# Kernel optimization log

Hardware: AMD Instinct MI355X
Metric: run time of the kernel (lower is better)

The kernel has to match this reference:

```python
import jax, jax.numpy as jnp
import numpy as np

B, N, DIM = 32, 577, 768   # N = num_patches + 1
H, DH = 12, 64             # heads, dim_head; inner_dim = H*DH = 768
NEG = -987654321.0         # LSA diagonal mask value from the source


def setup_inputs() -> dict:
    key = jax.random.key(0)
    ks = jax.random.split(key, 5)
    inner = H * DH
    base_scale = DH ** -0.5
    return {
        "x": jax.random.normal(ks[0], (B, N, DIM), dtype=jnp.float32),
        "W_qkv": jax.random.normal(ks[1], (DIM, inner * 3), dtype=jnp.float32) * (DIM ** -0.5),
        "scale": base_scale * (1.0 + 0.01 * jax.random.normal(ks[2], (H,), dtype=jnp.float32)),
        "W_out": jax.random.normal(ks[3], (inner, DIM), dtype=jnp.float32) * (inner ** -0.5),
        "b_out": jnp.zeros((DIM,), dtype=jnp.float32),
    }


def reference(x, W_qkv, scale, W_out, b_out):
    b, n, _ = x.shape
    qkv = x @ W_qkv                                   # [b, n, 3*H*DH]
    q, k, v = jnp.split(qkv, 3, axis=-1)
    to_heads = lambda t: t.reshape(b, n, H, DH).transpose(0, 2, 1, 3)  # b h n d
    q, k, v = to_heads(q), to_heads(k), to_heads(v)
    # per-head learnable scale (LSA)
    dots = jnp.einsum('bhid,bhjd->bhij', q, k) * scale[None, :, None, None]
    # mask self-attention diagonal (eye scatter in the torch source)
    eye = jnp.eye(n, dtype=bool)
    dots = jnp.where(eye[None, None], NEG, dots)
    attn = jax.nn.softmax(dots, axis=-1)
    out = jnp.einsum('bhij,bhjd->bhid', attn, v)      # b h n d
    out = out.transpose(0, 2, 1, 3).reshape(b, n, H * DH)
    return out @ W_out + b_out
```

## Files before the change

kernel.cpp:

```cpp
#include <hip/hip_runtime.h>


typedef _Float16 half8  __attribute__((ext_vector_type(8)));
typedef _Float16 h4f    __attribute__((ext_vector_type(4)));
typedef __fp16   hv2    __attribute__((ext_vector_type(2)));
typedef __fp16   hv4    __attribute__((ext_vector_type(4)));
typedef float    floatx4 __attribute__((ext_vector_type(4)));

#define MTOT   18464
#define NEG_V  (-987654321.0f)
#define VTS    584

__device__ __forceinline__ void gl_lds16(const _Float16* g, _Float16* l) {
    __builtin_amdgcn_global_load_lds(
        (const __attribute__((address_space(1))) unsigned int*)g,
        (__attribute__((address_space(3))) unsigned int*)l,
        16, 0, 0);
}

__global__ __launch_bounds__(256) void cvt_x(const float* __restrict__ x,
                                             _Float16* __restrict__ x16) {
    const size_t idx = ((size_t)blockIdx.x * 256 + threadIdx.x) * 8;
    half8 h = {};
    if (idx < (size_t)MTOT * 768) {
        float4 a = *(const float4*)(x + idx);
        float4 b = *(const float4*)(x + idx + 4);
        h[0] = (_Float16)a.x; h[1] = (_Float16)a.y;
        h[2] = (_Float16)a.z; h[3] = (_Float16)a.w;
        h[4] = (_Float16)b.x; h[5] = (_Float16)b.y;
        h[6] = (_Float16)b.z; h[7] = (_Float16)b.w;
    }
    *(half8*)(x16 + idx) = h;
}

__global__ __launch_bounds__(256) void transpose_w(const float* __restrict__ src,
                                                   _Float16* __restrict__ dst,
                                                   int K, int Ncol) {
    __shared__ float tile[32][33];
    const int n0 = blockIdx.x * 32, k0 = blockIdx.y * 32;
    const int tx = threadIdx.x & 31, ty = threadIdx.x >> 5;
    for (int i = 0; i < 32; i += 8)
        tile[ty + i][tx] = src[(size_t)(k0 + ty + i) * Ncol + (n0 + tx)];
    __syncthreads();
    for (int i = 0; i < 32; i += 8)
        dst[(size_t)(n0 + ty + i) * K + (k0 + tx)] = (_Float16)tile[tx][ty + i];
}

__global__ __launch_bounds__(512, 4) void gemm_qkv(const _Float16* __restrict__ x16,
                                                   const _Float16* __restrict__ wT,
                                                   const float* __restrict__ scale,
                                                   _Float16* __restrict__ qg,
                                                   _Float16* __restrict__ kg,
                                                   _Float16* __restrict__ vT) {
    __shared__ _Float16 As[2][128 * 32];
    __shared__ _Float16 Bs[2][256 * 32];
    const int m0 = blockIdx.x * 128, n0 = blockIdx.y * 256;
    const int tid = threadIdx.x;
    const int lane = tid & 63, wv = tid >> 6;
    const int wrow = wv >> 2, wcol = wv & 3;
    const int lr = lane & 15, lq = lane >> 4;

    const int ra  = tid >> 2,            ca  = (tid & 3) * 8;
    const int rb0 = tid >> 2,            cb0 = (tid & 3) * 8;
    const int rb1 = (512 + tid) >> 2,    cb1 = (tid & 3) * 8;

    floatx4 acc[4][4];
    const floatx4 fz = {0.f, 0.f, 0.f, 0.f};
    for (int i = 0; i < 4; ++i)
        for (int j = 0; j < 4; ++j) acc[i][j] = fz;

    #define STAGE_QKV(ki, bf)                                                     \
        do {                                                                      \
            const int kk_ = (ki) * 32;                                            \
            gl_lds16(x16 + (size_t)(m0 + ra) * 768 + kk_ + ca, &As[bf][wv*64*8]); \
            gl_lds16(wT + (size_t)(n0 + rb0) * 768 + kk_ + cb0, &Bs[bf][wv*64*8]);\
            gl_lds16(wT + (size_t)(n0 + rb1) * 768 + kk_ + cb1,                   \
                     &Bs[bf][(512 + wv*64) * 8]);                                 \
        } while (0)

    STAGE_QKV(0, 0);
    for (int ki = 0; ki < 24; ++ki) {
        const int bf = ki & 1;
        if (ki < 23) {
            STAGE_QKV(ki + 1, bf ^ 1);
            asm volatile("s_waitcnt vmcnt(3)" ::: "memory");
        } else {
            asm volatile("s_waitcnt vmcnt(0)" ::: "memory");
        }
        asm volatile("s_barrier" ::: "memory");

        half8 af[4], bfr[4];
        #pragma unroll
        for (int i = 0; i < 4; ++i)
            af[i] = *(const half8*)&As[bf][(wrow * 64 + i * 16 + lr) * 32 + lq * 8];
        #pragma unroll
        for (int j = 0; j < 4; ++j)
            bfr[j] = *(const half8*)&Bs[bf][(wcol * 64 + j * 16 + lr) * 32 + lq * 8];
        #pragma unroll
        for (int i = 0; i < 4; ++i)
            #pragma unroll
            for (int j = 0; j < 4; ++j)
                acc[i][j] = __builtin_amdgcn_mfma_f32_16x16x32_f16(af[i], bfr[j], acc[i][j], 0, 0, 0);

        asm volatile("s_waitcnt lgkmcnt(0)\n\ts_barrier" ::: "memory");
    }
    #undef STAGE_QKV

    const int cbase = n0 + wcol * 64;
    const int which = cbase / 768;
    const int h = (cbase - which * 768) >> 6;
    const float qsc = (which == 0) ? scale[h] * 1.4426950408889634f : 1.0f;
    #pragma unroll
    for (int j = 0; j < 4; ++j) {
        const int d = j * 16 + lr;
        #pragma unroll
        for (int i = 0; i < 4; ++i)
            #pragma unroll
            for (int r = 0; r < 4; ++r) {
                const int row = m0 + wrow * 64 + i * 16 + lq * 4 + r;
                if (row >= MTOT) continue;
                const unsigned bb = (unsigned)row / 577u;
                const unsigned nn = (unsigned)row - bb * 577u;
                const _Float16 val = (_Float16)(acc[i][j][r] * qsc);
                const size_t head = (size_t)(bb * 12 + h);
                if (which == 0)      qg[(head * 577 + nn) * 64 + d] = val;
                else if (which == 1) kg[(head * 577 + nn) * 64 + d] = val;
                else                 vT[(head * 64 + d) * VTS + nn] = val;
            }
    }
}

__global__ __launch_bounds__(256) void attn_kernel(const _Float16* __restrict__ qg,
                                                   const _Float16* __restrict__ kg,
                                                   const _Float16* __restrict__ vT,
                                                   _Float16* __restrict__ Og) {
    __shared__ __align__(16) _Float16 Ks[64 * 64];
    __shared__ __align__(16) _Float16 Vs[64 * 64];
    const int qt = blockIdx.x, h = blockIdx.y, b = blockIdx.z;
    const int tid = threadIdx.x, lane = tid & 63, wv = tid >> 6;
    const int lr = lane & 15, lq = lane >> 4;
    const size_t head = (size_t)(b * 12 + h);
    const _Float16* qh = qg + head * 577 * 64;
    const _Float16* kh = kg + head * 577 * 64;
    const _Float16* vh = vT + head * 64 * VTS;
    const int q0 = qt * 128;
    const int xs = lq ^ (lr & 7), xs4 = xs ^ 4;

    half8 bq[2][2];
    #pragma unroll
    for (int st = 0; st < 2; ++st) {
        const int qi = q0 + st * 64 + wv * 16 + lr;
        const int qc = qi < 577 ? qi : 576;
        bq[st][0] = *(const half8*)(qh + (size_t)qc * 64 + lq * 8);
        bq[st][1] = *(const half8*)(qh + (size_t)qc * 64 + 32 + lq * 8);
    }

    const floatx4 fz = {0.f, 0.f, 0.f, 0.f};
    floatx4 ot[2][4];
    #pragma unroll
    for (int st = 0; st < 2; ++st)
        #pragma unroll
        for (int c = 0; c < 4; ++c) ot[st][c] = fz;
    float sacc[2] = {0.f, 0.f};

    for (int kt = 0; kt < 10; ++kt) {
        const int j0 = kt * 64;
        __syncthreads();
        #pragma unroll
        for (int t = 0; t < 2; ++t) {
            const int c = t * 256 + wv * 64 + lane;
            const int row = c >> 3, cl = (c & 7) ^ (row & 7);
            gl_lds16(kh + (size_t)(j0 + row) * 64 + cl * 8,
                     Ks + (t * 256 + wv * 64) * 8);
            gl_lds16(vh + (size_t)row * VTS + j0 + cl * 8,
                     Vs + (t * 256 + wv * 64) * 8);
        }
        __syncthreads();

        half8 ak[4][2];
        #pragma unroll
        for (int ct = 0; ct < 4; ++ct) {
            const int base = (ct * 16 + lr) * 64;
            ak[ct][0] = *(const half8*)&Ks[base + xs * 8];
            ak[ct][1] = *(const half8*)&Ks[base + xs4 * 8];
        }

        floatx4 s[2][4];
        #pragma unroll
        for (int st = 0; st < 2; ++st)
            #pragma unroll
            for (int ct = 0; ct < 4; ++ct) {
                floatx4 t = __builtin_amdgcn_mfma_f32_16x16x32_f16(ak[ct][0], bq[st][0], fz, 0, 0, 0);
                s[st][ct] = __builtin_amdgcn_mfma_f32_16x16x32_f16(ak[ct][1], bq[st][1], t, 0, 0, 0);
            }

        if (kt == 9) {
            #pragma unroll
            for (int st = 0; st < 2; ++st) {
                s[st][0][0] = (lq == 0) ? s[st][0][0] : -INFINITY;
                s[st][0][1] = -INFINITY; s[st][0][2] = -INFINITY; s[st][0][3] = -INFINITY;
                #pragma unroll
                for (int ct = 1; ct < 4; ++ct) {
                    s[st][ct][0] = -INFINITY; s[st][ct][1] = -INFINITY;
                    s[st][ct][2] = -INFINITY; s[st][ct][3] = -INFINITY;
                }
            }
        }
        #pragma unroll
        for (int st = 0; st < 2; ++st) {
            if (kt == qt * 2 + st) {
                #pragma unroll
                for (int ct = 0; ct < 4; ++ct)
                    if (ct == wv) {
                        #pragma unroll
                        for (int r = 0; r < 4; ++r)
                            if (lq * 4 + r == lr) s[st][ct][r] = -INFINITY;
                    }
            }
        }

        hv4 pk[2][4];
        #pragma unroll
        for (int st = 0; st < 2; ++st)
            #pragma unroll
            for (int ct = 0; ct < 4; ++ct) {
                const float p0 = __builtin_amdgcn_exp2f(s[st][ct][0]);
                const float p1 = __builtin_amdgcn_exp2f(s[st][ct][1]);
                const float p2 = __builtin_amdgcn_exp2f(s[st][ct][2]);
                const float p3 = __builtin_amdgcn_exp2f(s[st][ct][3]);
                sacc[st] += (p0 + p1) + (p2 + p3);
                const hv2 lo = __builtin_amdgcn_cvt_pkrtz(p0, p1);
                const hv2 hi = __builtin_amdgcn_cvt_pkrtz(p2, p3);
                pk[st][ct] = __builtin_shufflevector(lo, hi, 0, 1, 2, 3);
            }

        #pragma unroll
        for (int jc = 0; jc < 4; ++jc) {
            const int csv = ((jc << 1) | (lq >> 1)) ^ (lr & 7);
            #pragma unroll
            for (int ctd = 0; ctd < 4; ++ctd) {
                const hv4 av = *(const hv4*)&Vs[(ctd * 16 + lr) * 64 + csv * 8 + (lq & 1) * 4];
                #pragma unroll
                for (int st = 0; st < 2; ++st)
                    ot[st][ctd] = __builtin_amdgcn_mfma_f32_16x16x16f16(av, pk[st][jc], ot[st][ctd], 0, 0, 0);
            }
        }
    }

    #pragma unroll
    for (int st = 0; st < 2; ++st) {
        float l = sacc[st];
        l += __shfl_xor(l, 16, 64);
        l += __shfl_xor(l, 32, 64);
        const float linv = 1.f / l;
        const int i = q0 + st * 64 + wv * 16 + lr;
        if (i < 577) {
            #pragma unroll
            for (int ctd = 0; ctd < 4; ++ctd) {
                h4f ov;
                #pragma unroll
                for (int r = 0; r < 4; ++r) ov[r] = (_Float16)(ot[st][ctd][r] * linv);
                *(h4f*)(Og + ((size_t)(b * 577 + i)) * 768 + h * 64 + ctd * 16 + lq * 4) = ov;
            }
        }
    }
}

__global__ __launch_bounds__(512, 4) void gemm_out(const _Float16* __restrict__ Og,
                                                   const _Float16* __restrict__ wT,
                                                   const float* __restrict__ bias,
                                                   float* __restrict__ out) {
    __shared__ _Float16 As[2][128 * 32];
    __shared__ _Float16 Bs[2][256 * 32];
    const int m0 = blockIdx.x * 128, n0 = blockIdx.y * 256;
    const int tid = threadIdx.x;
    const int lane = tid & 63, wv = tid >> 6;
    const int wrow = wv >> 2, wcol = wv & 3;
    const int lr = lane & 15, lq = lane >> 4;

    const int ra  = tid >> 2,         ca  = (tid & 3) * 8;
    const int rb0 = tid >> 2,         cb0 = (tid & 3) * 8;
    const int rb1 = (512 + tid) >> 2, cb1 = (tid & 3) * 8;

    floatx4 acc[4][4];
    const floatx4 fz = {0.f, 0.f, 0.f, 0.f};
    for (int i = 0; i < 4; ++i)
        for (int j = 0; j < 4; ++j) acc[i][j] = fz;

    #define STAGE_OUT(ki, bf)                                                     \
        do {                                                                      \
            const int kk_ = (ki) * 32;                                            \
            gl_lds16(Og + (size_t)(m0 + ra) * 768 + kk_ + ca, &As[bf][wv*64*8]);  \
            gl_lds16(wT + (size_t)(n0 + rb0) * 768 + kk_ + cb0, &Bs[bf][wv*64*8]);\
            gl_lds16(wT + (size_t)(n0 + rb1) * 768 + kk_ + cb1,                   \
                     &Bs[bf][(512 + wv*64) * 8]);                                 \
        } while (0)

    STAGE_OUT(0, 0);
    for (int ki = 0; ki < 24; ++ki) {
        const int bf = ki & 1;
        if (ki < 23) {
            STAGE_OUT(ki + 1, bf ^ 1);
            asm volatile("s_waitcnt vmcnt(3)" ::: "memory");
        } else {
            asm volatile("s_waitcnt vmcnt(0)" ::: "memory");
        }
        asm volatile("s_barrier" ::: "memory");

        half8 af[4], bfr[4];
        #pragma unroll
        for (int i = 0; i < 4; ++i)
            af[i] = *(const half8*)&As[bf][(wrow * 64 + i * 16 + lr) * 32 + lq * 8];
        #pragma unroll
        for (int j = 0; j < 4; ++j)
            bfr[j] = *(const half8*)&Bs[bf][(wcol * 64 + j * 16 + lr) * 32 + lq * 8];
        #pragma unroll
        for (int i = 0; i < 4; ++i)
            #pragma unroll
            for (int j = 0; j < 4; ++j)
                acc[i][j] = __builtin_amdgcn_mfma_f32_16x16x32_f16(af[i], bfr[j], acc[i][j], 0, 0, 0);

        asm volatile("s_waitcnt lgkmcnt(0)\n\ts_barrier" ::: "memory");
    }
    #undef STAGE_OUT

    #pragma unroll
    for (int j = 0; j < 4; ++j) {
        const int c = n0 + wcol * 64 + j * 16 + lr;
        const float bv = bias[c];
        #pragma unroll
        for (int i = 0; i < 4; ++i)
            #pragma unroll
            for (int r = 0; r < 4; ++r) {
                const int row = m0 + wrow * 64 + i * 16 + lq * 4 + r;
                if (row < MTOT) out[(size_t)row * 768 + c] = acc[i][j][r] + bv;
            }
    }
}

extern "C" void kernel_launch(void* const* d_in, const int* in_sizes, int n_in,
                              void* d_out, int out_size, void* d_ws, size_t ws_size,
                              hipStream_t stream) {
    const float* x      = (const float*)d_in[0];
    const float* W_qkv  = (const float*)d_in[1];
    const float* scale  = (const float*)d_in[2];
    const float* W_out  = (const float*)d_in[3];
    const float* b_out  = (const float*)d_in[4];
    float* out = (float*)d_out;

    char* ws = (char*)d_ws;
    _Float16* x16   = (_Float16*)(ws);
    _Float16* Og    = x16;
    _Float16* qg    = (_Float16*)(ws + 28508160u);
    _Float16* kg    = (_Float16*)(ws + 28508160u + 28360704u);
    _Float16* vT    = (_Float16*)(ws + 28508160u + 2u * 28360704u);
    _Float16* WqkvT = (_Float16*)(ws + 28508160u + 2u * 28360704u + 28704768u);
    _Float16* WoutT = WqkvT + (size_t)2304 * 768;

    cvt_x<<<6960, 256, 0, stream>>>(x, x16);
    transpose_w<<<dim3(72, 24), 256, 0, stream>>>(W_qkv, WqkvT, 768, 2304);
    transpose_w<<<dim3(24, 24), 256, 0, stream>>>(W_out, WoutT, 768, 768);
    gemm_qkv<<<dim3(145, 9), 512, 0, stream>>>(x16, WqkvT, scale, qg, kg, vT);
    attn_kernel<<<dim3(5, 12, 32), 256, 0, stream>>>(qg, kg, vT, Og);
    gemm_out<<<dim3(145, 3), 512, 0, stream>>>(Og, WoutT, b_out, out);
}
```

Baseline: 352.1 us.

## Add XCD-aware block swizzle, LDS XOR swizzle in GEMMs, and MFMA priority hints

Flattens the grids of all three main kernels and remaps block indices so consecutive tiles land on the same XCD, improving L2 reuse of shared weight and K/V data. The two GEMMs also apply an XOR swizzle to the LDS column chunk on both the global-to-LDS store and the fragment reads, to cut LDS bank conflicts. The attention kernel raises wave priority around its MFMA blocks with s_setprio. The swizzle math relies on the exact grid sizes (1305, 435, 1920) and adds integer divides per block.

```diff
diff --git a/kernel.cpp b/kernel.cpp
--- a/kernel.cpp
+++ b/kernel.cpp
@@ -54,28 +54,33 @@
                                                    _Float16* __restrict__ vT) {
     __shared__ _Float16 As[2][128 * 32];
     __shared__ _Float16 Bs[2][256 * 32];
-    const int m0 = blockIdx.x * 128, n0 = blockIdx.y * 256;
+    const unsigned orig = blockIdx.x;
+    const unsigned xcd = orig & 7u, bidx = orig >> 3;
+    const unsigned swz = (xcd == 0u ? 0u : 164u + (xcd - 1u) * 163u) + bidx;
+    const unsigned mi = swz / 9u, ni = swz - mi * 9u;
+    const int m0 = (int)mi * 128, n0 = (int)ni * 256;
     const int tid = threadIdx.x;
     const int lane = tid & 63, wv = tid >> 6;
     const int wrow = wv >> 2, wcol = wv & 3;
     const int lr = lane & 15, lq = lane >> 4;
 
-    const int ra  = tid >> 2,            ca  = (tid & 3) * 8;
-    const int rb0 = tid >> 2,            cb0 = (tid & 3) * 8;
-    const int rb1 = (512 + tid) >> 2,    cb1 = (tid & 3) * 8;
+    const int ra  = tid >> 2,         ca  = (((tid & 3) ^ ((ra  >> 1) & 3)) * 8);
+    const int rb0 = tid >> 2,         cb0 = (((tid & 3) ^ ((rb0 >> 1) & 3)) * 8);
+    const int rb1 = (512 + tid) >> 2, cb1 = (((tid & 3) ^ ((rb1 >> 1) & 3)) * 8);
+    const int xc = (lq ^ ((lr >> 1) & 3)) * 8;
 
     floatx4 acc[4][4];
     const floatx4 fz = {0.f, 0.f, 0.f, 0.f};
     for (int i = 0; i < 4; ++i)
         for (int j = 0; j < 4; ++j) acc[i][j] = fz;
 
-    #define STAGE_QKV(ki, bf)                                                     \
-        do {                                                                      \
-            const int kk_ = (ki) * 32;                                            \
-            gl_lds16(x16 + (size_t)(m0 + ra) * 768 + kk_ + ca, &As[bf][wv*64*8]); \
-            gl_lds16(wT + (size_t)(n0 + rb0) * 768 + kk_ + cb0, &Bs[bf][wv*64*8]);\
-            gl_lds16(wT + (size_t)(n0 + rb1) * 768 + kk_ + cb1,                   \
-                     &Bs[bf][(512 + wv*64) * 8]);                                 \
+    #define STAGE_QKV(ki, bfx)                                                     \
+        do {                                                                       \
+            const int kk_ = (ki) * 32;                                             \
+            gl_lds16(x16 + (size_t)(m0 + ra) * 768 + kk_ + ca, &As[bfx][wv*64*8]); \
+            gl_lds16(wT + (size_t)(n0 + rb0) * 768 + kk_ + cb0, &Bs[bfx][wv*64*8]);\
+            gl_lds16(wT + (size_t)(n0 + rb1) * 768 + kk_ + cb1,                    \
+                     &Bs[bfx][(512 + wv*64) * 8]);                                 \
         } while (0)
 
     STAGE_QKV(0, 0);
@@ -92,10 +97,10 @@
         half8 af[4], bfr[4];
         #pragma unroll
         for (int i = 0; i < 4; ++i)
-            af[i] = *(const half8*)&As[bf][(wrow * 64 + i * 16 + lr) * 32 + lq * 8];
+            af[i] = *(const half8*)&As[bf][(wrow * 64 + i * 16 + lr) * 32 + xc];
         #pragma unroll
         for (int j = 0; j < 4; ++j)
-            bfr[j] = *(const half8*)&Bs[bf][(wcol * 64 + j * 16 + lr) * 32 + lq * 8];
+            bfr[j] = *(const half8*)&Bs[bf][(wcol * 64 + j * 16 + lr) * 32 + xc];
         #pragma unroll
         for (int i = 0; i < 4; ++i)
             #pragma unroll
@@ -136,7 +141,11 @@
                                                    _Float16* __restrict__ Og) {
     __shared__ __align__(16) _Float16 Ks[64 * 64];
     __shared__ __align__(16) _Float16 Vs[64 * 64];
-    const int qt = blockIdx.x, h = blockIdx.y, b = blockIdx.z;
+    const unsigned orig = blockIdx.x;
+    const unsigned swz = (orig & 7u) * 240u + (orig >> 3);
+    const int qt = (int)(swz % 5u);
+    const unsigned hb = swz / 5u;
+    const int h = (int)(hb % 12u), b = (int)(hb / 12u);
     const int tid = threadIdx.x, lane = tid & 63, wv = tid >> 6;
     const int lr = lane & 15, lq = lane >> 4;
     const size_t head = (size_t)(b * 12 + h);
@@ -186,6 +195,7 @@
         }
 
         floatx4 s[2][4];
+        __builtin_amdgcn_s_setprio(1);
         #pragma unroll
         for (int st = 0; st < 2; ++st)
             #pragma unroll
@@ -193,6 +203,7 @@
                 floatx4 t = __builtin_amdgcn_mfma_f32_16x16x32_f16(ak[ct][0], bq[st][0], fz, 0, 0, 0);
                 s[st][ct] = __builtin_amdgcn_mfma_f32_16x16x32_f16(ak[ct][1], bq[st][1], t, 0, 0, 0);
             }
+        __builtin_amdgcn_s_setprio(0);
 
         if (kt == 9) {
             #pragma unroll
@@ -234,6 +245,7 @@
                 pk[st][ct] = __builtin_shufflevector(lo, hi, 0, 1, 2, 3);
             }
 
+        __builtin_amdgcn_s_setprio(1);
         #pragma unroll
         for (int jc = 0; jc < 4; ++jc) {
             const int csv = ((jc << 1) | (lq >> 1)) ^ (lr & 7);
@@ -245,6 +257,7 @@
                     ot[st][ctd] = __builtin_amdgcn_mfma_f32_16x16x16f16(av, pk[st][jc], ot[st][ctd], 0, 0, 0);
             }
         }
+        __builtin_amdgcn_s_setprio(0);
     }
 
     #pragma unroll
@@ -272,28 +285,33 @@
                                                    float* __restrict__ out) {
     __shared__ _Float16 As[2][128 * 32];
     __shared__ _Float16 Bs[2][256 * 32];
-    const int m0 = blockIdx.x * 128, n0 = blockIdx.y * 256;
+    const unsigned orig = blockIdx.x;
+    const unsigned xcd = orig & 7u, bidx = orig >> 3;
+    const unsigned swz = (xcd < 3u ? xcd * 55u : 165u + (xcd - 3u) * 54u) + bidx;
+    const unsigned mi = swz / 3u, ni = swz - mi * 3u;
+    const int m0 = (int)mi * 128, n0 = (int)ni * 256;
     const int tid = threadIdx.x;
     const int lane = tid & 63, wv = tid >> 6;
     const int wrow = wv >> 2, wcol = wv & 3;
     const int lr = lane & 15, lq = lane >> 4;
 
-    const int ra  = tid >> 2,         ca  = (tid & 3) * 8;
-    const int rb0 = tid >> 2,         cb0 = (tid & 3) * 8;
-    const int rb1 = (512 + tid) >> 2, cb1 = (tid & 3) * 8;
+    const int ra  = tid >> 2,         ca  = (((tid & 3) ^ ((ra  >> 1) & 3)) * 8);
+    const int rb0 = tid >> 2,         cb0 = (((tid & 3) ^ ((rb0 >> 1) & 3)) * 8);
+    const int rb1 = (512 + tid) >> 2, cb1 = (((tid & 3) ^ ((rb1 >> 1) & 3)) * 8);
+    const int xc = (lq ^ ((lr >> 1) & 3)) * 8;
 
     floatx4 acc[4][4];
     const floatx4 fz = {0.f, 0.f, 0.f, 0.f};
     for (int i = 0; i < 4; ++i)
         for (int j = 0; j < 4; ++j) acc[i][j] = fz;
 
-    #define STAGE_OUT(ki, bf)                                                     \
-        do {                                                                      \
-            const int kk_ = (ki) * 32;                                            \
-            gl_lds16(Og + (size_t)(m0 + ra) * 768 + kk_ + ca, &As[bf][wv*64*8]);  \
-            gl_lds16(wT + (size_t)(n0 + rb0) * 768 + kk_ + cb0, &Bs[bf][wv*64*8]);\
-            gl_lds16(wT + (size_t)(n0 + rb1) * 768 + kk_ + cb1,                   \
-                     &Bs[bf][(512 + wv*64) * 8]);                                 \
+    #define STAGE_OUT(ki, bfx)                                                     \
+        do {                                                                       \
+            const int kk_ = (ki) * 32;                                             \
+            gl_lds16(Og + (size_t)(m0 + ra) * 768 + kk_ + ca, &As[bfx][wv*64*8]);  \
+            gl_lds16(wT + (size_t)(n0 + rb0) * 768 + kk_ + cb0, &Bs[bfx][wv*64*8]);\
+            gl_lds16(wT + (size_t)(n0 + rb1) * 768 + kk_ + cb1,                    \
+                     &Bs[bfx][(512 + wv*64) * 8]);                                 \
         } while (0)
 
     STAGE_OUT(0, 0);
@@ -310,10 +328,10 @@
         half8 af[4], bfr[4];
         #pragma unroll
         for (int i = 0; i < 4; ++i)
-            af[i] = *(const half8*)&As[bf][(wrow * 64 + i * 16 + lr) * 32 + lq * 8];
+            af[i] = *(const half8*)&As[bf][(wrow * 64 + i * 16 + lr) * 32 + xc];
         #pragma unroll
         for (int j = 0; j < 4; ++j)
-            bfr[j] = *(const half8*)&Bs[bf][(wcol * 64 + j * 16 + lr) * 32 + lq * 8];
+            bfr[j] = *(const half8*)&Bs[bf][(wcol * 64 + j * 16 + lr) * 32 + xc];
         #pragma unroll
         for (int i = 0; i < 4; ++i)
             #pragma unroll
@@ -360,7 +378,7 @@
     cvt_x<<<6960, 256, 0, stream>>>(x, x16);
     transpose_w<<<dim3(72, 24), 256, 0, stream>>>(W_qkv, WqkvT, 768, 2304);
     transpose_w<<<dim3(24, 24), 256, 0, stream>>>(W_out, WoutT, 768, 768);
-    gemm_qkv<<<dim3(145, 9), 512, 0, stream>>>(x16, WqkvT, scale, qg, kg, vT);
-    attn_kernel<<<dim3(5, 12, 32), 256, 0, stream>>>(qg, kg, vT, Og);
-    gemm_out<<<dim3(145, 3), 512, 0, stream>>>(Og, WoutT, b_out, out);
-}
+    gemm_qkv<<<1305, 512, 0, stream>>>(x16, WqkvT, scale, qg, kg, vT);
+    attn_kernel<<<1920, 256, 0, stream>>>(qg, kg, vT, Og);
+    gemm_out<<<435, 512, 0, stream>>>(Og, WoutT, b_out, out);
+}
```

After: 358.4 us. Within noise of the previous version (+1.8%).
